# Kernel tuning notes

Hardware: AMD Instinct MI355X
Metric: run time of the kernel (lower is better)

The kernel has to match this reference:

```python
import jax, jax.numpy as jnp
import numpy as np

NUM_USERS = 100000
NUM_ITEMS = 50000
N = NUM_USERS + NUM_ITEMS
EMB = 64
N_LAYERS = 3
N_EDGES = 4800000
BATCH = 4096


def setup_inputs() -> dict:
    key = jax.random.key(0)
    ks = jax.random.split(key, 8)
    users = jax.random.randint(ks[0], (BATCH,), 0, NUM_USERS, dtype=jnp.int64 if jax.config.jax_enable_x64 else jnp.int32)
    pos_items = jax.random.randint(ks[1], (BATCH,), 0, NUM_ITEMS)
    neg_items = jax.random.randint(ks[2], (BATCH,), 0, NUM_ITEMS)
    adj_rows = jax.random.randint(ks[3], (N_EDGES,), 0, N)
    adj_cols = jax.random.randint(ks[4], (N_EDGES,), 0, N)
    # scale values like a degree-normalized adjacency (~1/deg) to keep magnitudes stable
    adj_vals = jax.random.uniform(ks[5], (N_EDGES,), dtype=jnp.float32) * (1.0 / 32.0)
    user_emb = jax.random.normal(ks[6], (NUM_USERS, EMB), dtype=jnp.float32) * 0.1
    item_emb = jax.random.normal(ks[7], (NUM_ITEMS, EMB), dtype=jnp.float32) * 0.1
    return {"users": users, "pos_items": pos_items, "neg_items": neg_items,
            "adj_rows": adj_rows, "adj_cols": adj_cols, "adj_vals": adj_vals,
            "user_emb": user_emb, "item_emb": item_emb}


def _spmm(rows, cols, vals, x):
    # sparse (N,N) @ dense (N,E): gather columns, scale, scatter-add to rows
    gathered = x[cols] * vals[:, None]          # [n_edges, EMB]
    return jax.ops.segment_sum(gathered, rows, num_segments=N)


def reference(users, pos_items, neg_items, adj_rows, adj_cols, adj_vals, user_emb, item_emb):
    emb = jnp.concatenate([user_emb, item_emb], axis=0)  # [N, EMB]
    acc = emb
    cur = emb
    for _ in range(N_LAYERS):
        cur = _spmm(adj_rows, adj_cols, adj_vals, cur)
        acc = acc + cur
    final = acc / (N_LAYERS + 1)                # layer-wise mean
    users_emb = final[:NUM_USERS]
    items_emb = final[NUM_USERS:]
    u = users_emb[users]                        # [B, EMB]
    pos = items_emb[pos_items]
    neg = items_emb[neg_items]
    pos_scores = jnp.sum(u * pos, axis=1)       # [B]
    neg_scores = jnp.sum(u * neg, axis=1)
    return (pos_scores, neg_scores)
```

## Files before the change

### kernel.cpp

```cpp
#include <hip/hip_runtime.h>

#define NUM_USERS 100000
#define NUM_ITEMS 50000
#define NNODES    150000
#define EMB       64
#define NEDGES    4800000
#define BATCH     4096
#define BUCKETS   293
#define BROWS     512
#define EPB       8192
#define NBLK_A    586
#define CAP       17408
#define INIT_BLKS 2344
#define NSAMP     (3 * BATCH)

typedef unsigned short u16;
typedef unsigned int   u32;

__device__ inline float bf2f(u16 u) { return __uint_as_float(((u32)u) << 16); }
__device__ inline u16 f2bf(float f) {
    u32 b = __float_as_uint(f);
    b += 0x7FFFu + ((b >> 16) & 1u);
    return (u16)(b >> 16);
}
__device__ inline u32 pack2(float a, float b) {
    return (u32)f2bf(a) | ((u32)f2bf(b) << 16);
}

__device__ inline void init_body(const float* __restrict__ user_emb,
                                 const float* __restrict__ item_emb,
                                 u16* __restrict__ l0, long i) {
    const long n4 = (long)NNODES * EMB / 4;
    if (i >= n4) return;
    const long nu4 = (long)NUM_USERS * EMB / 4;
    float4 v = (i < nu4) ? ((const float4*)user_emb)[i]
                         : ((const float4*)item_emb)[i - nu4];
    ushort4 o;
    o.x = f2bf(v.x); o.y = f2bf(v.y); o.z = f2bf(v.z); o.w = f2bf(v.w);
    ((ushort4*)l0)[i] = o;
}

__global__ void init_kernel(const float* __restrict__ user_emb,
                            const float* __restrict__ item_emb,
                            u16* __restrict__ l0) {
    init_body(user_emb, item_emb, l0, (long)blockIdx.x * blockDim.x + threadIdx.x);
}

__global__ void __launch_bounds__(512) binA_kernel(const int* __restrict__ rows,
                                                   const int* __restrict__ cols,
                                                   const float* __restrict__ vals,
                                                   int* __restrict__ bfill,
                                                   int2* __restrict__ tmp,
                                                   const float* __restrict__ uemb,
                                                   const float* __restrict__ iemb,
                                                   u16* __restrict__ l0) {
    if (blockIdx.x >= NBLK_A) {
        long ib = blockIdx.x - NBLK_A;
        long i = ib * 1024 + threadIdx.x;
        init_body(uemb, iemb, l0, i);
        init_body(uemb, iemb, l0, i + 512);
        return;
    }
    __shared__ int hist[BUCKETS];
    __shared__ int cursor[BUCKETS];
    const int tid = threadIdx.x;
    for (int i = tid; i < BUCKETS; i += 512) hist[i] = 0;
    __syncthreads();

    const long base = (long)blockIdx.x * EPB;
    #pragma unroll
    for (int k = 0; k < 16; ++k) {
        long e = base + (long)k * 512 + tid;
        if (e < NEDGES) atomicAdd(&hist[rows[e] >> 9], 1);
    }
    __syncthreads();

    for (int b = tid; b < BUCKETS; b += 512) {
        int h = hist[b];
        cursor[b] = h ? b * CAP + atomicAdd(&bfill[b], h) : 0;
    }
    __syncthreads();

    #pragma unroll
    for (int k = 0; k < 16; ++k) {
        long e = base + (long)k * 512 + tid;
        if (e < NEDGES) {
            int r = rows[e];
            int pos = atomicAdd(&cursor[r >> 9], 1);
            tmp[pos] = make_int2(((r & 511) << 18) | cols[e], __float_as_int(vals[e]));
        }
    }
}

__global__ void scan_buckets(const int* __restrict__ bfill, int* __restrict__ bucketBase) {
    int lane = threadIdx.x;
    int carry = 0;
    for (int cb = 0; cb < BUCKETS; cb += 64) {
        int i = cb + lane;
        int orig = (i < BUCKETS) ? bfill[i] : 0;
        int x = orig;
        #pragma unroll
        for (int d = 1; d < 64; d <<= 1) {
            int t = __shfl_up(x, d, 64);
            if (lane >= d) x += t;
        }
        int total = __shfl(x, 63, 64);
        if (i < BUCKETS) bucketBase[i] = x - orig + carry;
        carry += total;
    }
}

__global__ void __launch_bounds__(512) binB_kernel(const int* __restrict__ bfill,
                                                   const int* __restrict__ bucketBase,
                                                   const int2* __restrict__ tmp,
                                                   int* __restrict__ rowPtr,
                                                   int2* __restrict__ csr) {
    const int bucket = blockIdx.x;
    __shared__ int lhist[BROWS];
    __shared__ int rp[BROWS];
    __shared__ int fill[BROWS];
    const int t = threadIdx.x;
    lhist[t] = 0; fill[t] = 0;
    __syncthreads();

    const int cnt = bfill[bucket];
    const int2* src = tmp + (long)bucket * CAP;
    for (int k = t; k < cnt; k += 512)
        atomicAdd(&lhist[src[k].x >> 18], 1);
    __syncthreads();

    const int gb = bucketBase[bucket];
    if (t < 64) {
        int carry = 0;
        for (int cb = 0; cb < BROWS; cb += 64) {
            int i = cb + t;
            int orig = lhist[i];
            int x = orig;
            #pragma unroll
            for (int d = 1; d < 64; d <<= 1) {
                int tt = __shfl_up(x, d, 64);
                if (t >= d) x += tt;
            }
            int total = __shfl(x, 63, 64);
            rp[i] = x - orig + carry + gb;
            carry += total;
        }
    }
    __syncthreads();

    int rowIdx = bucket * BROWS + t;
    rowPtr[rowIdx] = rp[t];

    for (int k = t; k < cnt; k += 512) {
        int2 p = src[k];
        int rL = p.x >> 18;
        int pos = rp[rL] + atomicAdd(&fill[rL], 1);
        csr[pos] = make_int2(p.x & 0x3FFFF, p.y);
    }
}

#define ACCX(V, X) { \
    a[0] += (V) * __uint_as_float((X).x << 16); \
    a[1] += (V) * __uint_as_float((X).x & 0xFFFF0000u); \
    a[2] += (V) * __uint_as_float((X).y << 16); \
    a[3] += (V) * __uint_as_float((X).y & 0xFFFF0000u); \
    a[4] += (V) * __uint_as_float((X).z << 16); \
    a[5] += (V) * __uint_as_float((X).z & 0xFFFF0000u); \
    a[6] += (V) * __uint_as_float((X).w << 16); \
    a[7] += (V) * __uint_as_float((X).w & 0xFFFF0000u); }

__global__ void spmm_csr(const int* __restrict__ rowPtr, const int2* __restrict__ csr,
                         const u16* __restrict__ cur, u16* __restrict__ nxt) {
    int gtid = blockIdx.x * blockDim.x + threadIdx.x;
    int row = gtid >> 3;
    int t   = gtid & 7;
    if (row >= NNODES) return;
    int beg = rowPtr[row], end = rowPtr[row + 1];
    float a[8];
    #pragma unroll
    for (int i = 0; i < 8; ++i) a[i] = 0.f;

    int e = beg;
    for (; e + 7 < end; e += 8) {
        int2 p[8];
        #pragma unroll
        for (int j = 0; j < 8; ++j) p[j] = csr[e + j];
        uint4 x[8];
        #pragma unroll
        for (int j = 0; j < 8; ++j)
            x[j] = *(const uint4*)(cur + ((long)p[j].x << 6) + (t << 3));
        #pragma unroll
        for (int j = 0; j < 8; ++j) {
            float v = __int_as_float(p[j].y);
            ACCX(v, x[j]);
        }
    }
    for (; e < end; ++e) {
        int2 p = csr[e];
        float v = __int_as_float(p.y);
        uint4 x = *(const uint4*)(cur + ((long)p.x << 6) + (t << 3));
        ACCX(v, x);
    }

    uint4 o;
    o.x = pack2(a[0], a[1]);
    o.y = pack2(a[2], a[3]);
    o.z = pack2(a[4], a[5]);
    o.w = pack2(a[6], a[7]);
    *(uint4*)(nxt + ((long)row << 6) + (t << 3)) = o;
}

__global__ void spmm_sampled(const int* __restrict__ users,
                             const int* __restrict__ pos_items,
                             const int* __restrict__ neg_items,
                             const int* __restrict__ rowPtr, const int2* __restrict__ csr,
                             const u16* __restrict__ cur, float* __restrict__ sampled) {
    int gtid = blockIdx.x * blockDim.x + threadIdx.x;
    int slot = gtid >> 3;
    int t    = gtid & 7;
    if (slot >= NSAMP) return;
    int row;
    if (slot < BATCH)          row = users[slot];
    else if (slot < 2 * BATCH) row = pos_items[slot - BATCH] + NUM_USERS;
    else                       row = neg_items[slot - 2 * BATCH] + NUM_USERS;

    int beg = rowPtr[row], end = rowPtr[row + 1];
    float a[8];
    #pragma unroll
    for (int i = 0; i < 8; ++i) a[i] = 0.f;

    int e = beg;
    for (; e + 7 < end; e += 8) {
        int2 p[8];
        #pragma unroll
        for (int j = 0; j < 8; ++j) p[j] = csr[e + j];
        uint4 x[8];
        #pragma unroll
        for (int j = 0; j < 8; ++j)
            x[j] = *(const uint4*)(cur + ((long)p[j].x << 6) + (t << 3));
        #pragma unroll
        for (int j = 0; j < 8; ++j) {
            float v = __int_as_float(p[j].y);
            ACCX(v, x[j]);
        }
    }
    for (; e < end; ++e) {
        int2 p = csr[e];
        float v = __int_as_float(p.y);
        uint4 x = *(const uint4*)(cur + ((long)p.x << 6) + (t << 3));
        ACCX(v, x);
    }

    float4* dst = (float4*)(sampled + ((long)slot << 6) + (t << 3));
    dst[0] = make_float4(a[0], a[1], a[2], a[3]);
    dst[1] = make_float4(a[4], a[5], a[6], a[7]);
}

__global__ void score_kernel(const int* __restrict__ users,
                             const int* __restrict__ pos_items,
                             const int* __restrict__ neg_items,
                             const float* __restrict__ uemb,
                             const float* __restrict__ iemb,
                             const u16* __restrict__ l1,
                             const u16* __restrict__ l2,
                             const float* __restrict__ sampled,
                             float* __restrict__ out) {
    int gtid = blockIdx.x * blockDim.x + threadIdx.x;
    int wave = gtid >> 6;
    int lane = threadIdx.x & 63;
    if (wave >= BATCH) return;
    int u = users[wave];
    int p = pos_items[wave];
    int n = neg_items[wave];
    long U = (long)u * EMB + lane;
    long P = (long)(p + NUM_USERS) * EMB + lane;
    long N = (long)(n + NUM_USERS) * EMB + lane;
    float ue = uemb[(long)u * EMB + lane] + bf2f(l1[U]) + bf2f(l2[U])
             + sampled[(long)wave * EMB + lane];
    float pe = iemb[(long)p * EMB + lane] + bf2f(l1[P]) + bf2f(l2[P])
             + sampled[(long)(BATCH + wave) * EMB + lane];
    float ne = iemb[(long)n * EMB + lane] + bf2f(l1[N]) + bf2f(l2[N])
             + sampled[(long)(2 * BATCH + wave) * EMB + lane];
    float ps = ue * pe;
    float ns = ue * ne;
    #pragma unroll
    for (int off = 32; off > 0; off >>= 1) {
        ps += __shfl_down(ps, off, 64);
        ns += __shfl_down(ns, off, 64);
    }
    if (lane == 0) {
        out[wave]         = ps * 0.0625f;
        out[BATCH + wave] = ns * 0.0625f;
    }
}

extern "C" void kernel_launch(void* const* d_in, const int* in_sizes, int n_in,
                              void* d_out, int out_size, void* d_ws, size_t ws_size,
                              hipStream_t stream) {
    const int*   users = (const int*)d_in[0];
    const int*   pos   = (const int*)d_in[1];
    const int*   neg   = (const int*)d_in[2];
    const int*   rows  = (const int*)d_in[3];
    const int*   cols  = (const int*)d_in[4];
    const float* vals  = (const float*)d_in[5];
    const float* uemb  = (const float*)d_in[6];
    const float* iemb  = (const float*)d_in[7];
    float* out = (float*)d_out;

    const size_t tblElems = (size_t)NNODES * EMB;
    u16*  B0      = (u16*)d_ws;
    u16*  B1      = B0 + tblElems;
    u16*  B2      = B1 + tblElems;
    int2* csr     = (int2*)(B2 + tblElems);
    int*  rowPtr  = (int*)(csr + NEDGES);
    int*  bfill   = rowPtr + 150016;
    int*  bucketB = bfill + 320;
    float* sampled= (float*)(bucketB + 320);
    int*  tailEnd = (int*)(sampled + (size_t)NSAMP * EMB);

    const size_t tmpBytes = (size_t)BUCKETS * CAP * sizeof(int2);
    const size_t baseBytes = (size_t)((char*)tailEnd - (char*)d_ws);
    const bool  bigws = ws_size >= baseBytes + tmpBytes;
    int2* tmp = bigws ? (int2*)tailEnd : (int2*)B0;

    hipMemsetAsync(bfill, 0, 320 * sizeof(int), stream);

    int gridA = NBLK_A + (bigws ? INIT_BLKS : 0);
    binA_kernel<<<gridA, 512, 0, stream>>>(rows, cols, vals, bfill, tmp,
                                           uemb, iemb, B0);
    scan_buckets<<<1, 64, 0, stream>>>(bfill, bucketB);
    binB_kernel<<<BUCKETS, 512, 0, stream>>>(bfill, bucketB, tmp, rowPtr, csr);

    if (!bigws) {
        const long n4 = (long)tblElems / 4;
        init_kernel<<<(int)((n4 + 255) / 256), 256, 0, stream>>>(uemb, iemb, B0);
    }

    const long nth = (long)NNODES * 8;
    const int  spmmGrid = (int)((nth + 255) / 256);
    spmm_csr<<<spmmGrid, 256, 0, stream>>>(rowPtr, csr, B0, B1);
    spmm_csr<<<spmmGrid, 256, 0, stream>>>(rowPtr, csr, B1, B2);
    spmm_sampled<<<(NSAMP * 8 + 255) / 256, 256, 0, stream>>>(users, pos, neg,
                                                              rowPtr, csr, B2, sampled);

    score_kernel<<<(BATCH * 64) / 256, 256, 0, stream>>>(users, pos, neg,
                                                         uemb, iemb, B1, B2, sampled, out);
}
```

Baseline: 482.4 us.

## Stage binned edges in shared memory and write them to global contiguously per bucket

The first binning pass now does a local prefix scan over its bucket histogram and scatters edges into a 64KB shared-memory buffer. Whole waves then copy each bucket's run to global memory, replacing scattered per-thread global writes with coalesced bursts. Row indices are kept in registers so rows are not reloaded. The init work is no longer fused into binA and runs as a separate launch, and tmp now always gets a dedicated workspace region. The large shared allocation cuts occupancy, and the workspace requirement grows.

```diff
diff --git a/kernel.cpp b/kernel.cpp
--- a/kernel.cpp
+++ b/kernel.cpp
@@ -11,7 +11,6 @@
 #define EPB       8192
 #define NBLK_A    586
 #define CAP       17408
-#define INIT_BLKS 2344
 #define NSAMP     (3 * BATCH)
 
 typedef unsigned short u16;
@@ -27,9 +26,10 @@
     return (u32)f2bf(a) | ((u32)f2bf(b) << 16);
 }
 
-__device__ inline void init_body(const float* __restrict__ user_emb,
-                                 const float* __restrict__ item_emb,
-                                 u16* __restrict__ l0, long i) {
+__global__ void init_kernel(const float* __restrict__ user_emb,
+                            const float* __restrict__ item_emb,
+                            u16* __restrict__ l0) {
+    long i = (long)blockIdx.x * blockDim.x + threadIdx.x;
     const long n4 = (long)NNODES * EMB / 4;
     if (i >= n4) return;
     const long nu4 = (long)NUM_USERS * EMB / 4;
@@ -40,55 +40,78 @@
     ((ushort4*)l0)[i] = o;
 }
 
-__global__ void init_kernel(const float* __restrict__ user_emb,
-                            const float* __restrict__ item_emb,
-                            u16* __restrict__ l0) {
-    init_body(user_emb, item_emb, l0, (long)blockIdx.x * blockDim.x + threadIdx.x);
-}
-
 __global__ void __launch_bounds__(512) binA_kernel(const int* __restrict__ rows,
                                                    const int* __restrict__ cols,
                                                    const float* __restrict__ vals,
                                                    int* __restrict__ bfill,
-                                                   int2* __restrict__ tmp,
-                                                   const float* __restrict__ uemb,
-                                                   const float* __restrict__ iemb,
-                                                   u16* __restrict__ l0) {
-    if (blockIdx.x >= NBLK_A) {
-        long ib = blockIdx.x - NBLK_A;
-        long i = ib * 1024 + threadIdx.x;
-        init_body(uemb, iemb, l0, i);
-        init_body(uemb, iemb, l0, i + 512);
-        return;
-    }
-    __shared__ int hist[BUCKETS];
-    __shared__ int cursor[BUCKETS];
+                                                   int2* __restrict__ tmp) {
+    __shared__ int2 ebuf[EPB];
+    __shared__ int  hist[BUCKETS];
+    __shared__ int  start[BUCKETS];
+    __shared__ int  cursor[BUCKETS];
+    __shared__ int  gbase[BUCKETS];
     const int tid = threadIdx.x;
     for (int i = tid; i < BUCKETS; i += 512) hist[i] = 0;
     __syncthreads();
 
     const long base = (long)blockIdx.x * EPB;
+    int rsave[16];
     #pragma unroll
     for (int k = 0; k < 16; ++k) {
         long e = base + (long)k * 512 + tid;
-        if (e < NEDGES) atomicAdd(&hist[rows[e] >> 9], 1);
+        int r = -1;
+        if (e < NEDGES) {
+            r = rows[e];
+            atomicAdd(&hist[r >> 9], 1);
+        }
+        rsave[k] = r;
+    }
+    __syncthreads();
+
+    if (tid < 64) {
+        int carry = 0;
+        for (int cb = 0; cb < BUCKETS; cb += 64) {
+            int i = cb + tid;
+            int orig = (i < BUCKETS) ? hist[i] : 0;
+            int x = orig;
+            #pragma unroll
+            for (int d = 1; d < 64; d <<= 1) {
+                int t = __shfl_up(x, d, 64);
+                if (tid >= d) x += t;
+            }
+            int total = __shfl(x, 63, 64);
+            if (i < BUCKETS) { start[i] = x - orig + carry; cursor[i] = x - orig + carry; }
+            carry += total;
+        }
     }
     __syncthreads();
 
     for (int b = tid; b < BUCKETS; b += 512) {
         int h = hist[b];
-        cursor[b] = h ? b * CAP + atomicAdd(&bfill[b], h) : 0;
-    }
-    __syncthreads();
+        gbase[b] = h ? b * CAP + atomicAdd(&bfill[b], h) : 0;
+    }
 
     #pragma unroll
     for (int k = 0; k < 16; ++k) {
-        long e = base + (long)k * 512 + tid;
-        if (e < NEDGES) {
-            int r = rows[e];
+        int r = rsave[k];
+        if (r >= 0) {
+            long e = base + (long)k * 512 + tid;
             int pos = atomicAdd(&cursor[r >> 9], 1);
-            tmp[pos] = make_int2(((r & 511) << 18) | cols[e], __float_as_int(vals[e]));
-        }
+            ebuf[pos] = make_int2(((r & 511) << 18) | cols[e], __float_as_int(vals[e]));
+        }
+    }
+    __syncthreads();
+
+    const int wv = tid >> 6, lane = tid & 63;
+    const int* eb32 = (const int*)ebuf;
+    int* gtmp = (int*)tmp;
+    for (int b = wv; b < BUCKETS; b += 8) {
+        int cnt2 = hist[b] * 2;
+        if (!cnt2) continue;
+        int  s2 = start[b] * 2;
+        long d2 = (long)gbase[b] * 2;
+        for (int i = lane; i < cnt2; i += 64)
+            gtmp[d2 + i] = eb32[s2 + i];
     }
 }
 
@@ -311,30 +334,21 @@
     u16*  B0      = (u16*)d_ws;
     u16*  B1      = B0 + tblElems;
     u16*  B2      = B1 + tblElems;
-    int2* csr     = (int2*)(B2 + tblElems);
+    int2* tmp     = (int2*)(B2 + tblElems);
+    int2* csr     = (int2*)(tmp + (size_t)BUCKETS * CAP);
     int*  rowPtr  = (int*)(csr + NEDGES);
     int*  bfill   = rowPtr + 150016;
     int*  bucketB = bfill + 320;
     float* sampled= (float*)(bucketB + 320);
-    int*  tailEnd = (int*)(sampled + (size_t)NSAMP * EMB);
-
-    const size_t tmpBytes = (size_t)BUCKETS * CAP * sizeof(int2);
-    const size_t baseBytes = (size_t)((char*)tailEnd - (char*)d_ws);
-    const bool  bigws = ws_size >= baseBytes + tmpBytes;
-    int2* tmp = bigws ? (int2*)tailEnd : (int2*)B0;
 
     hipMemsetAsync(bfill, 0, 320 * sizeof(int), stream);
 
-    int gridA = NBLK_A + (bigws ? INIT_BLKS : 0);
-    binA_kernel<<<gridA, 512, 0, stream>>>(rows, cols, vals, bfill, tmp,
-                                           uemb, iemb, B0);
+    binA_kernel<<<NBLK_A, 512, 0, stream>>>(rows, cols, vals, bfill, tmp);
     scan_buckets<<<1, 64, 0, stream>>>(bfill, bucketB);
     binB_kernel<<<BUCKETS, 512, 0, stream>>>(bfill, bucketB, tmp, rowPtr, csr);
 
-    if (!bigws) {
-        const long n4 = (long)tblElems / 4;
-        init_kernel<<<(int)((n4 + 255) / 256), 256, 0, stream>>>(uemb, iemb, B0);
-    }
+    const long n4 = (long)tblElems / 4;
+    init_kernel<<<(int)((n4 + 255) / 256), 256, 0, stream>>>(uemb, iemb, B0);
 
     const long nth = (long)NNODES * 8;
     const int  spmmGrid = (int)((nth + 255) / 256);
```

After: 456.5 us. 5.4% less time.
